# Kernel optimization log

Measured on AMD Instinct MI355X. Metric: run time of the kernel, lower is better.

Reference implementation:

```python
import jax, jax.numpy as jnp
import numpy as np

N = 200000   # 10000 graphs x 20 nodes, stacked
E = 3200000  # avg degree 16
F_IN = 4
H = 32
BN_EPS = 1e-5


def setup_inputs() -> dict:
    key = jax.random.key(0)
    ks = jax.random.split(key, 16)
    s = 0.1
    return {
        "x": jax.random.normal(ks[0], (N, F_IN), jnp.float32),
        "edge_index": jax.random.randint(ks[1], (2, E), 0, N, jnp.int64),
        "edge_weight": jax.random.uniform(ks[2], (E,), jnp.float32),
        "gcn1_w": jax.random.normal(ks[3], (F_IN, H), jnp.float32) * s,
        "gcn1_b": jnp.zeros((H,), jnp.float32),
        "gcn2_w": jax.random.normal(ks[4], (H, H), jnp.float32) * s,
        "gcn2_b": jnp.zeros((H,), jnp.float32),
        "bn1_gamma": jnp.ones((H,), jnp.float32),
        "bn1_beta": jnp.zeros((H,), jnp.float32),
        "bn1_mean": jnp.zeros((H,), jnp.float32),
        "bn1_var": jnp.ones((H,), jnp.float32),
        "bn2_gamma": jnp.ones((H,), jnp.float32),
        "bn2_beta": jnp.zeros((H,), jnp.float32),
        "bn2_mean": jnp.zeros((H,), jnp.float32),
        "bn2_var": jnp.ones((H,), jnp.float32),
        "lstm1_wih": jax.random.normal(ks[5], (4 * H, 2 * H), jnp.float32) * s,
        "lstm1_whh": jax.random.normal(ks[6], (4 * H, H), jnp.float32) * s,
        "lstm1_bih": jax.random.normal(ks[7], (4 * H,), jnp.float32) * s,
        "lstm1_bhh": jax.random.normal(ks[8], (4 * H,), jnp.float32) * s,
        "lstm2_wih": jax.random.normal(ks[9], (4 * H, H), jnp.float32) * s,
        "lstm2_whh": jax.random.normal(ks[10], (4 * H, H), jnp.float32) * s,
        "lstm2_bih": jax.random.normal(ks[11], (4 * H,), jnp.float32) * s,
        "lstm2_bhh": jax.random.normal(ks[12], (4 * H,), jnp.float32) * s,
        "lin_w": jax.random.normal(ks[13], (1, 2 * H + F_IN), jnp.float32) * s,
        "lin_b": jnp.zeros((1,), jnp.float32),
    }


def _gcn_conv(x, src, dst, ew, W, b, n):
    # GCNConv: x @ W, add self-loops (weight 1), symmetric normalization, scatter-add at dst.
    xw = x @ W
    loop = jnp.arange(n)
    s = jnp.concatenate([src, loop])
    d = jnp.concatenate([dst, loop])
    w = jnp.concatenate([ew, jnp.ones((n,), ew.dtype)])
    deg = jax.ops.segment_sum(w, d, num_segments=n)
    dinv = jnp.where(deg > 0, jax.lax.rsqrt(deg), 0.0)
    norm = dinv[s] * w * dinv[d]  # [E+N]
    out = jax.ops.segment_sum(norm[:, None] * xw[s], d, num_segments=n)
    return out + b


def _bn_eval(x, gamma, beta, mean, var):
    return (x - mean) * jax.lax.rsqrt(var + BN_EPS) * gamma + beta


def _lstm_step(x, wih, bih, bhh):
    # single timestep, zero initial (h, c): recurrent W_hh term vanishes.
    gates = x @ wih.T + bih + bhh
    i, f, g, o = jnp.split(gates, 4, axis=1)  # torch gate order i,f,g,o
    c = jax.nn.sigmoid(i) * jnp.tanh(g)
    return jax.nn.sigmoid(o) * jnp.tanh(c)


def reference(x, edge_index, edge_weight, gcn1_w, gcn1_b, gcn2_w, gcn2_b,
              bn1_gamma, bn1_beta, bn1_mean, bn1_var,
              bn2_gamma, bn2_beta, bn2_mean, bn2_var,
              lstm1_wih, lstm1_whh, lstm1_bih, lstm1_bhh,
              lstm2_wih, lstm2_whh, lstm2_bih, lstm2_bhh,
              lin_w, lin_b):
    n = x.shape[0]
    src, dst = edge_index[0], edge_index[1]
    # MPNNLSTM (window=1, eval mode: dropout=identity, BN uses running stats)
    h1 = _bn_eval(jax.nn.relu(_gcn_conv(x, src, dst, edge_weight, gcn1_w, gcn1_b, n)),
                  bn1_gamma, bn1_beta, bn1_mean, bn1_var)
    h2 = _bn_eval(jax.nn.relu(_gcn_conv(h1, src, dst, edge_weight, gcn2_w, gcn2_b, n)),
                  bn2_gamma, bn2_beta, bn2_mean, bn2_var)
    skip = jnp.concatenate([h1, h2], axis=1)  # [N, 2H]
    H1 = _lstm_step(skip, lstm1_wih, lstm1_bih, lstm1_bhh)  # [N, H]
    H2 = _lstm_step(H1, lstm2_wih, lstm2_bih, lstm2_bhh)    # [N, H]
    h = jnp.concatenate([H1, H2, x], axis=1)  # [N, 2H + F_IN]
    # RecurrentGCN head: relu + linear -> [N, 1]
    return jax.nn.relu(h) @ lin_w.T + lin_b
```

## Files before the change

kernel.cpp:

```cpp
#include <hip/hip_runtime.h>
#include <hip/hip_fp16.h>
#include <math.h>

#define BN_EPS 1e-5f
#define HF 32
#define BS 256
#define KEDGE 4096
#define MAXNB 800
#define SCAP 5504
#define WQ14 16383.0f
#define WQ22 4194303.0f

typedef _Float16 half8 __attribute__((ext_vector_type(8)));
typedef float f32x4 __attribute__((ext_vector_type(4)));
typedef float f32x2 __attribute__((ext_vector_type(2)));

__device__ __forceinline__ float fsig(float x) {
    return __builtin_amdgcn_rcpf(1.0f + __expf(-x));
}
__device__ __forceinline__ float ftanh(float x) {
    return 1.0f - 2.0f * __builtin_amdgcn_rcpf(1.0f + __expf(2.0f * x));
}


__device__ __forceinline__ float e4m3_to_f32_sw(unsigned v) {
    unsigned s = v & 0x80u, E = (v >> 3) & 0xFu, m = v & 7u;
    float r = E ? ldexpf((float)(8 + m), (int)E - 10) : ldexpf((float)m, -9);
    return s ? -r : r;
}

__device__ __forceinline__ unsigned f32_to_e4m3_sw(float x) {
    float ax = fabsf(x);
    unsigned s = x < 0.0f ? 0x80u : 0u;
    if (!(ax > 0.0f)) return s;
    if (ax >= 448.0f) return s | 0x7Eu;
    int e;
    float m = frexpf(ax, &e);
    int E = e - 1 + 7;
    if (E >= 1) {
        int q = (int)(m * 16.0f + 0.5f);
        if (q == 16) { q = 8; E += 1; if (E > 15) return s | 0x7Eu; }
        return s | (unsigned)(E << 3) | (unsigned)(q - 8);
    }
    int q = (int)(ax * 512.0f + 0.5f);
    if (q > 7) return s | 0x08u;
    return s | (unsigned)q;
}

__device__ __forceinline__ void dec8(uint2 r, float* f) {
#if __has_builtin(__builtin_amdgcn_cvt_pk_f32_fp8)
    f32x2 p0 = __builtin_amdgcn_cvt_pk_f32_fp8((int)r.x, false);
    f32x2 p1 = __builtin_amdgcn_cvt_pk_f32_fp8((int)r.x, true);
    f32x2 p2 = __builtin_amdgcn_cvt_pk_f32_fp8((int)r.y, false);
    f32x2 p3 = __builtin_amdgcn_cvt_pk_f32_fp8((int)r.y, true);
    f[0] = p0[0]; f[1] = p0[1]; f[2] = p1[0]; f[3] = p1[1];
    f[4] = p2[0]; f[5] = p2[1]; f[6] = p3[0]; f[7] = p3[1];
#else
#pragma unroll
    for (int k = 0; k < 4; ++k) f[k] = e4m3_to_f32_sw((r.x >> (8 * k)) & 0xFFu);
#pragma unroll
    for (int k = 0; k < 4; ++k) f[4 + k] = e4m3_to_f32_sw((r.y >> (8 * k)) & 0xFFu);
#endif
}

__device__ __forceinline__ uint2 enc8(const float* o) {
#if __has_builtin(__builtin_amdgcn_cvt_pk_fp8_f32)
    int w0 = 0, w1 = 0;
    w0 = __builtin_amdgcn_cvt_pk_fp8_f32(o[0], o[1], w0, false);
    w0 = __builtin_amdgcn_cvt_pk_fp8_f32(o[2], o[3], w0, true);
    w1 = __builtin_amdgcn_cvt_pk_fp8_f32(o[4], o[5], w1, false);
    w1 = __builtin_amdgcn_cvt_pk_fp8_f32(o[6], o[7], w1, true);
    return make_uint2((unsigned)w0, (unsigned)w1);
#else
    unsigned a = 0, b = 0;
#pragma unroll
    for (int k = 0; k < 4; ++k) a |= f32_to_e4m3_sw(o[k]) << (8 * k);
#pragma unroll
    for (int k = 0; k < 4; ++k) b |= f32_to_e4m3_sw(o[4 + k]) << (8 * k);
    return make_uint2(a, b);
#endif
}


__global__ __launch_bounds__(512) void k_binsort(
        const int* __restrict__ src, const int* __restrict__ dst,
        const float* __restrict__ ew, int E, int NB, int bcap,
        int* __restrict__ gcur, uint2* __restrict__ recs) {
    __shared__ int hist[MAXNB], curs[MAXNB];

    int tid = threadIdx.x;
    int base = blockIdx.x * KEDGE;
    int cnt = min(KEDGE, E - base);

    for (int i = tid; i < NB; i += 512) hist[i] = 0;
    __syncthreads();

    uint2 rec[8];
    int eb = base + tid * 8;
    int rem = cnt - tid * 8;
    if (rem >= 8) {
        int4 s0 = *(const int4*)(src + eb);
        int4 s1 = *(const int4*)(src + eb + 4);
        int4 d0 = *(const int4*)(dst + eb);
        int4 d1 = *(const int4*)(dst + eb + 4);
        float4 w0 = *(const float4*)(ew + eb);
        float4 w1 = *(const float4*)(ew + eb + 4);
        int ss[8] = {s0.x, s0.y, s0.z, s0.w, s1.x, s1.y, s1.z, s1.w};
        int dd[8] = {d0.x, d0.y, d0.z, d0.w, d1.x, d1.y, d1.z, d1.w};
        float ww[8] = {w0.x, w0.y, w0.z, w0.w, w1.x, w1.y, w1.z, w1.w};
#pragma unroll
        for (int k = 0; k < 8; ++k) {
            unsigned q = (unsigned)(ww[k] * WQ22 + 0.5f);
            if (q > 4194303u) q = 4194303u;
            int b = dd[k] >> 8;
            rec[k] = make_uint2(((unsigned)ss[k] << 8) | (unsigned)(dd[k] & 255),
                                ((unsigned)b << 22) | q);
        }
    } else {
#pragma unroll
        for (int k = 0; k < 8; ++k) {
            if (k < rem) {
                int s = src[eb + k];
                int d = dst[eb + k];
                float w = ew[eb + k];
                unsigned q = (unsigned)(w * WQ22 + 0.5f);
                if (q > 4194303u) q = 4194303u;
                int b = d >> 8;
                rec[k] = make_uint2(((unsigned)s << 8) | (unsigned)(d & 255),
                                    ((unsigned)b << 22) | q);
            }
        }
    }
#pragma unroll
    for (int k = 0; k < 8; ++k)
        if (k < rem) atomicAdd(&hist[rec[k].y >> 22], 1);
    __syncthreads();

    for (int b = tid; b < NB; b += 512) {
        int len = hist[b];
        curs[b] = len ? atomicAdd(&gcur[b], len) : 0;
    }
    __syncthreads();

#pragma unroll
    for (int k = 0; k < 8; ++k) {
        if (k < rem) {
            uint2 u = rec[k];
            int b = u.y >> 22;
            int off = atomicAdd(&curs[b], 1);
            if (off < bcap) recs[(size_t)b * bcap + off] = u;
        }
    }
}


__global__ __launch_bounds__(1024) void k_sortb(
        const uint2* __restrict__ recs, const int* __restrict__ gcur,
        int bcap, int bcap4,
        const float* __restrict__ x, const float* __restrict__ W1,
        unsigned* __restrict__ recs4, int* __restrict__ pstart,
        int* __restrict__ pcnt, float* __restrict__ dinv,
        unsigned char* __restrict__ y18,
        const float* __restrict__ wih1, const float* __restrict__ bih1,
        const float* __restrict__ bhh1, const float* __restrict__ wih2,
        const float* __restrict__ bih2, const float* __restrict__ bhh2,
        __half* __restrict__ wp1, __half* __restrict__ wp2,
        float* __restrict__ bsum1, float* __restrict__ bsum2, int n) {
    __shared__ uint2 srec[SCAP];
    __shared__ int hist[BS], excl4[BS], curs[BS], wsm[BS];
    __shared__ float sdv[BS];
    __shared__ float sW1[128];

    int b = blockIdx.x, tid = threadIdx.x;
    int cnt = min(gcur[b], bcap);
    const uint2* r = recs + (size_t)b * bcap;
    const float dq = 1.0f / WQ22;

    if (b == 0) {
        const int tg[6] = {0, 16, 64, 80, 96, 112};
        for (int idx = tid; idx < 9472; idx += 1024) {
            if (idx < 6144) {
                int t = idx >> 10, rm = idx & 1023;
                int kc = rm >> 9, rm2 = rm & 511;
                int lane = rm2 >> 3, j = rm2 & 7;
                int g = tg[t] + (lane & 15);
                int k = kc * 32 + (lane >> 4) * 8 + j;
                wp1[idx] = __float2half(wih1[g * 64 + k]);
            } else if (idx < 9216) {
                int i2 = idx - 6144;
                int t = i2 >> 9, rm2 = i2 & 511;
                int lane = rm2 >> 3, j = rm2 & 7;
                int g = tg[t] + (lane & 15);
                int k = (lane >> 4) * 8 + j;
                wp2[i2] = __float2half(wih2[g * 32 + k]);
            } else if (idx < 9344) {
                int i = idx - 9216;
                bsum1[i] = bih1[i] + bhh1[i];
            } else {
                int i = idx - 9344;
                bsum2[i] = bih2[i] + bhh2[i];
            }
        }
    }

    if (tid < BS) { hist[tid] = 0; wsm[tid] = 0; }
    if (tid >= 256 && tid < 384) sW1[tid - 256] = W1[tid - 256];
    __syncthreads();

    for (int i = tid; i < cnt; i += 1024) {
        uint2 u = r[i];
        if (i < SCAP) srec[i] = u;
        int dl = u.x & 255;
        atomicAdd(&hist[dl], 1);
        atomicAdd(&wsm[dl], (int)(u.y & 4194303u));
    }
    __syncthreads();

    if (tid < BS) {
        int g = b * BS + tid;
        sdv[tid] = (g < n) ? rsqrtf(1.0f + (float)wsm[tid] * dq) : 0.0f;
    }
    if (tid < 64) {
        int run = 0;
        for (int c = 0; c < BS; c += 64) {
            int idx = c + tid;
            int v = (hist[idx] + 3) & ~3;
            int incl = v;
#pragma unroll
            for (int o = 1; o < 64; o <<= 1) {
                int up = __shfl_up(incl, o, 64);
                if (tid >= o) incl += up;
            }
            int e = run + incl - v;
            excl4[idx] = e; curs[idx] = e;
            run += __shfl(incl, 63, 64);
        }
    }
    __syncthreads();

    unsigned* out4 = recs4 + (size_t)b * bcap4;
    for (int i = tid; i < cnt; i += 1024) {
        uint2 u = (i < SCAP) ? srec[i] : r[i];
        int dl = u.x & 255;
        int pos = atomicAdd(&curs[dl], 1);
        float qn = (float)(u.y & 4194303u) * dq * sdv[dl];
        unsigned q = (unsigned)(qn * WQ14 + 0.5f);
        if (q > 16383u) q = 16383u;
        out4[pos] = ((u.x >> 8) << 14) | q;
    }

    {
        int node = tid >> 2, q = tid & 3;
        int g = b * BS + node;
        if (g < n) {
            float4 xv = *(const float4*)(x + (size_t)g * 4);
            float sc = sdv[node];
            int f0 = q * 8;
            float o[8];
#pragma unroll
            for (int k = 0; k < 8; ++k)
                o[k] = sc * (xv.x * sW1[f0 + k] + xv.y * sW1[32 + f0 + k] +
                             xv.z * sW1[64 + f0 + k] + xv.w * sW1[96 + f0 + k]);
            ((uint2*)(y18 + ((size_t)g << 5)))[q] = enc8(o);
        }
    }

    if (tid < BS) {
        int g = b * BS + tid;
        if (g < n) {
            pstart[g] = b * bcap4 + excl4[tid];
            pcnt[g] = hist[tid];
            dinv[g] = sdv[tid];
        }
    }
}


__global__ __launch_bounds__(256) void k_g1w2(
        const unsigned* __restrict__ recs4, const int* __restrict__ pstart,
        const int* __restrict__ pcnt, const float* __restrict__ dinv,
        const unsigned char* __restrict__ y18, const float* __restrict__ W2,
        const float* __restrict__ bias, const float* __restrict__ gamma,
        const float* __restrict__ beta, const float* __restrict__ mean,
        const float* __restrict__ var,
        __half* __restrict__ skiph, unsigned char* __restrict__ A8, int n) {
    __shared__ float sW2[1024];
    __shared__ float sh1[64][33];
    int tid = threadIdx.x;
    for (int i = tid; i < 1024; i += 256) sW2[i] = W2[i];
    __syncthreads();

    int nl = tid >> 2;
    int g = blockIdx.x * 64 + nl;
    int lane = tid & 3;
    int fq = lane * 8;
    bool act = g < n;

    float acc[8];
#pragma unroll
    for (int k = 0; k < 8; ++k) acc[k] = 0.0f;

    float dig = 0.0f;
    if (act) {
        dig = dinv[g];
        {
            uint2 sr = ((const uint2*)(y18 + ((size_t)g << 5)))[lane];
            float f[8];
            dec8(sr, f);
#pragma unroll
            for (int k = 0; k < 8; ++k) acc[k] = dig * f[k];
        }

        const float qs = 1.0f / WQ14;
        int cn = pcnt[g];
        const unsigned* r = recs4 + pstart[g];
        uint4 na, nb;
        if (8 <= cn) { na = *(const uint4*)(r); nb = *(const uint4*)(r + 4); }
        int e = 0;
        for (; e + 8 <= cn; e += 8) {
            uint4 ua = na, ub = nb;
            if (e + 16 <= cn) { na = *(const uint4*)(r + e + 8); nb = *(const uint4*)(r + e + 12); }
            unsigned u[8] = {ua.x, ua.y, ua.z, ua.w, ub.x, ub.y, ub.z, ub.w};
            uint2 rw[8];
#pragma unroll
            for (int q = 0; q < 8; ++q)
                rw[q] = ((const uint2*)(y18 + ((size_t)(u[q] >> 14) << 5)))[lane];
            float nm[8];
#pragma unroll
            for (int q = 0; q < 8; ++q)
                nm[q] = (float)(u[q] & 16383u) * qs;
#pragma unroll
            for (int q = 0; q < 8; ++q) {
                float f[8];
                dec8(rw[q], f);
#pragma unroll
                for (int k = 0; k < 8; ++k) acc[k] += nm[q] * f[k];
            }
        }
        for (; e < cn; ++e) {
            unsigned u0 = r[e];
            uint2 r0 = ((const uint2*)(y18 + ((size_t)(u0 >> 14) << 5)))[lane];
            float n0 = (float)(u0 & 16383u) * qs;
            float f[8];
            dec8(r0, f);
#pragma unroll
            for (int k = 0; k < 8; ++k) acc[k] += n0 * f[k];
        }
    }

    float o[8];
#pragma unroll
    for (int k = 0; k < 8; ++k) {
        float v = fmaxf(acc[k] + bias[fq + k], 0.0f);
        o[k] = (v - mean[fq + k]) * gamma[fq + k] * rsqrtf(var[fq + k] + BN_EPS) + beta[fq + k];
        sh1[nl][fq + k] = o[k];
    }
    if (act) {
        union { __half h[8]; uint4 q; } hv;
#pragma unroll
        for (int k = 0; k < 8; ++k) hv.h[k] = __float2half(o[k]);
        *(uint4*)(skiph + (size_t)g * 32 + fq) = hv.q;
    }
    __syncthreads();

    if (act) {
        float a2[8];
#pragma unroll
        for (int j = 0; j < 8; ++j) a2[j] = 0.0f;
#pragma unroll 4
        for (int k = 0; k < 32; ++k) {
            float h = sh1[nl][k];
            const float* wr = sW2 + k * 32 + fq;
#pragma unroll
            for (int j = 0; j < 8; ++j) a2[j] += h * wr[j];
        }
#pragma unroll
        for (int j = 0; j < 8; ++j) a2[j] *= dig;
        ((uint2*)(A8 + ((size_t)g << 5)))[lane] = enc8(a2);
    }
}


__global__ __launch_bounds__(256) void k_g2head(
        const unsigned* __restrict__ recs4, const int* __restrict__ pstart,
        const int* __restrict__ pcnt, const float* __restrict__ dinv,
        const unsigned char* __restrict__ A8,
        const float* __restrict__ bias, const float* __restrict__ gamma,
        const float* __restrict__ beta, const float* __restrict__ mean,
        const float* __restrict__ var,
        const __half* __restrict__ skiph, const float* __restrict__ x,
        const __half* __restrict__ wp1, const __half* __restrict__ wp2,
        const float* __restrict__ bsum1, const float* __restrict__ bsum2,
        const float* __restrict__ lw, const float* __restrict__ lb,
        float* __restrict__ out, int n) {
    __shared__ __align__(16) __half h2s[64][40];
    __shared__ __align__(16) __half H1lds[4 * 16 * 40];
    int tid = threadIdx.x;
    int nl = tid >> 2;
    int g = blockIdx.x * 64 + nl;
    int lane = tid & 3;
    int fq = lane * 8;
    bool act = g < n;

    float acc[8];
#pragma unroll
    for (int k = 0; k < 8; ++k) acc[k] = 0.0f;

    if (act) {
        float dig = dinv[g];
        {
            uint2 sr = ((const uint2*)(A8 + ((size_t)g << 5)))[lane];
            float f[8];
            dec8(sr, f);
#pragma unroll
            for (int k = 0; k < 8; ++k) acc[k] = dig * f[k];
        }

        const float qs = 1.0f / WQ14;
        int cn = pcnt[g];
        const unsigned* r = recs4 + pstart[g];
        uint4 na, nb;
        if (8 <= cn) { na = *(const uint4*)(r); nb = *(const uint4*)(r + 4); }
        int e = 0;
        for (; e + 8 <= cn; e += 8) {
            uint4 ua = na, ub = nb;
            if (e + 16 <= cn) { na = *(const uint4*)(r + e + 8); nb = *(const uint4*)(r + e + 12); }
            unsigned u[8] = {ua.x, ua.y, ua.z, ua.w, ub.x, ub.y, ub.z, ub.w};
            uint2 rw[8];
#pragma unroll
            for (int q = 0; q < 8; ++q)
                rw[q] = ((const uint2*)(A8 + ((size_t)(u[q] >> 14) << 5)))[lane];
            float nm[8];
#pragma unroll
            for (int q = 0; q < 8; ++q)
                nm[q] = (float)(u[q] & 16383u) * qs;
#pragma unroll
            for (int q = 0; q < 8; ++q) {
                float f[8];
                dec8(rw[q], f);
#pragma unroll
                for (int k = 0; k < 8; ++k) acc[k] += nm[q] * f[k];
            }
        }
        for (; e < cn; ++e) {
            unsigned u0 = r[e];
            uint2 r0 = ((const uint2*)(A8 + ((size_t)(u0 >> 14) << 5)))[lane];
            float n0 = (float)(u0 & 16383u) * qs;
            float f0[8];
            dec8(r0, f0);
#pragma unroll
            for (int k = 0; k < 8; ++k) acc[k] += n0 * f0[k];
        }

        union { __half h[8]; uint4 q; } hv;
#pragma unroll
        for (int k = 0; k < 8; ++k) {
            float v = fmaxf(acc[k] + bias[fq + k], 0.0f);
            hv.h[k] = __float2half((v - mean[fq + k]) * gamma[fq + k] *
                                   rsqrtf(var[fq + k] + BN_EPS) + beta[fq + k]);
        }
        *(uint4*)(&h2s[nl][fq]) = hv.q;
    }
    __syncthreads();

    int w = tid >> 6, l = tid & 63;
    int quad = l >> 4, c = l & 15;
    int node_base = blockIdx.x * 64 + w * 16;

    int arow = node_base + c; if (arow > n - 1) arow = n - 1;
    int lr = arow - blockIdx.x * 64;
    half8 a0 = *(const half8*)(skiph + (size_t)arow * 32 + quad * 8);
    half8 a1 = *(const half8*)(&h2s[lr][quad * 8]);

    const half8* b1 = (const half8*)wp1;
    f32x4 d[6];
#pragma unroll
    for (int t = 0; t < 6; ++t) {
        f32x4 ac = {0.0f, 0.0f, 0.0f, 0.0f};
        ac = __builtin_amdgcn_mfma_f32_16x16x32_f16(a0, b1[(t * 2 + 0) * 64 + l], ac, 0, 0, 0);
        ac = __builtin_amdgcn_mfma_f32_16x16x32_f16(a1, b1[(t * 2 + 1) * 64 + l], ac, 0, 0, 0);
        d[t] = ac;
    }

    float bi0 = bsum1[c],      bi1 = bsum1[16 + c];
    float bg0 = bsum1[64 + c], bg1 = bsum1[80 + c];
    float bo0 = bsum1[96 + c], bo1 = bsum1[112 + c];
    float lwc0 = lw[c], lwc1 = lw[c + 16];

    float pa[4];
#pragma unroll
    for (int r = 0; r < 4; ++r) {
        float cc0 = fsig(d[0][r] + bi0) * ftanh(d[2][r] + bg0);
        float h0 = fsig(d[4][r] + bo0) * ftanh(cc0);
        float cc1 = fsig(d[1][r] + bi1) * ftanh(d[3][r] + bg1);
        float h1 = fsig(d[5][r] + bo1) * ftanh(cc1);
        pa[r] = fmaxf(h0, 0.0f) * lwc0 + fmaxf(h1, 0.0f) * lwc1;
        __half* hp = H1lds + (w * 16 + quad * 4 + r) * 40;
        hp[c] = __float2half(h0);
        hp[c + 16] = __float2half(h1);
    }
    __syncthreads();

    half8 a2 = *(const half8*)(H1lds + (w * 16 + c) * 40 + quad * 8);

    const half8* b2 = (const half8*)wp2;
    f32x4 e2[6];
#pragma unroll
    for (int t = 0; t < 6; ++t) {
        f32x4 ac = {0.0f, 0.0f, 0.0f, 0.0f};
        e2[t] = __builtin_amdgcn_mfma_f32_16x16x32_f16(a2, b2[t * 64 + l], ac, 0, 0, 0);
    }

    float ci0 = bsum2[c],      ci1 = bsum2[16 + c];
    float cg0 = bsum2[64 + c], cg1 = bsum2[80 + c];
    float co0 = bsum2[96 + c], co1 = bsum2[112 + c];
    float lw2c0 = lw[32 + c], lw2c1 = lw[48 + c];
#pragma unroll
    for (int r = 0; r < 4; ++r) {
        float cc0 = fsig(e2[0][r] + ci0) * ftanh(e2[2][r] + cg0);
        float h0 = fsig(e2[4][r] + co0) * ftanh(cc0);
        float cc1 = fsig(e2[1][r] + ci1) * ftanh(e2[3][r] + cg1);
        float h1 = fsig(e2[5][r] + co1) * ftanh(cc1);
        pa[r] += fmaxf(h0, 0.0f) * lw2c0 + fmaxf(h1, 0.0f) * lw2c1;
    }

#pragma unroll
    for (int m = 1; m < 16; m <<= 1) {
#pragma unroll
        for (int r = 0; r < 4; ++r) pa[r] += __shfl_xor(pa[r], m, 64);
    }

    if (c < 4) {
        int node = node_base + quad * 4 + c;
        if (node < n) {
            const float4 xv = *(const float4*)(x + (size_t)node * 4);
            out[node] = pa[c] + lb[0]
                + fmaxf(xv.x, 0.0f) * lw[64] + fmaxf(xv.y, 0.0f) * lw[65]
                + fmaxf(xv.z, 0.0f) * lw[66] + fmaxf(xv.w, 0.0f) * lw[67];
        }
    }
}


__global__ void k_initdeg(float* __restrict__ deg, int n) {
    int i = blockIdx.x * blockDim.x + threadIdx.x;
    if (i < n) deg[i] = 1.0f;
}

__global__ void k_deg_only(const int* __restrict__ dst, const float* __restrict__ ew,
                           float* __restrict__ deg, int E) {
    int e = blockIdx.x * blockDim.x + threadIdx.x;
    if (e < E) atomicAdd(&deg[dst[e]], ew[e]);
}

__global__ void k_dinv_f(float* __restrict__ deg, int n) {
    int i = blockIdx.x * blockDim.x + threadIdx.x;
    if (i < n) {
        float d = deg[i];
        deg[i] = d > 0.0f ? rsqrtf(d) : 0.0f;
    }
}

__global__ void k_xw1_f(const float* __restrict__ x, const float* __restrict__ W,
                        float* __restrict__ out, int n) {
    int idx = blockIdx.x * blockDim.x + threadIdx.x;
    if (idx >= n * HF) return;
    int nn = idx >> 5, f = idx & 31;
    const float4 xr = *(const float4*)(x + (size_t)nn * 4);
    out[idx] = xr.x * W[f] + xr.y * W[32 + f] + xr.z * W[64 + f] + xr.w * W[96 + f];
}

__global__ void k_xw2_f(const float* __restrict__ Hin, const float* __restrict__ W,
                        float* __restrict__ out, int n) {
    __shared__ float sW[32 * 32];
    __shared__ float sH[8][32];
    int tid = threadIdx.x;
    for (int i = tid; i < 1024; i += 256) sW[i] = W[i];
    int r = tid >> 5, f = tid & 31;
    int nn = blockIdx.x * 8 + r;
    if (nn < n) sH[r][f] = Hin[(size_t)nn * HF + f];
    __syncthreads();
    if (nn >= n) return;
    float acc = 0.0f;
#pragma unroll
    for (int k = 0; k < 32; ++k) acc += sH[r][k] * sW[k * 32 + f];
    out[(size_t)nn * HF + f] = acc;
}

__global__ void k_selfloop(const float* __restrict__ A, const float* __restrict__ dinv,
                           float* __restrict__ B, int n) {
    int idx = blockIdx.x * blockDim.x + threadIdx.x;
    if (idx >= n * HF) return;
    int nn = idx >> 5;
    float di = dinv[nn];
    B[idx] = di * di * A[idx];
}

__global__ void k_scatter(const int* __restrict__ src, const int* __restrict__ dst,
                          const float* __restrict__ ew, const float* __restrict__ dinv,
                          const float* __restrict__ A, float* __restrict__ B, int total) {
    int idx = blockIdx.x * blockDim.x + threadIdx.x;
    if (idx >= total) return;
    int e = idx >> 5, f = idx & 31;
    int s = src[e], d = dst[e];
    float norm = dinv[s] * ew[e] * dinv[d];
    atomicAdd(&B[d * HF + f], norm * A[s * HF + f]);
}

__global__ void k_post(const float* __restrict__ B, const float* __restrict__ bias,
                       const float* __restrict__ gamma, const float* __restrict__ beta,
                       const float* __restrict__ mean, const float* __restrict__ var,
                       float* __restrict__ Hout, int n) {
    int idx = blockIdx.x * blockDim.x + threadIdx.x;
    if (idx >= n * HF) return;
    int f = idx & 31;
    float v = fmaxf(B[idx] + bias[f], 0.0f);
    float sc = gamma[f] * rsqrtf(var[f] + BN_EPS);
    Hout[idx] = (v - mean[f]) * sc + beta[f];
}

__global__ __launch_bounds__(256) void k_head(
        const float* __restrict__ h1, const float* __restrict__ h2,
        const float* __restrict__ x,
        const float* __restrict__ wih1, const float* __restrict__ bih1, const float* __restrict__ bhh1,
        const float* __restrict__ wih2, const float* __restrict__ bih2, const float* __restrict__ bhh2,
        const float* __restrict__ lw, const float* __restrict__ lb,
        float* __restrict__ out, int n) {
    __shared__ float sH1[32 * 256];
    int tid = threadIdx.x;
    int nn = blockIdx.x * 256 + tid;
    if (nn >= n) return;

    const float4* a = (const float4*)(h1 + (size_t)nn * HF);
    const float4* b = (const float4*)(h2 + (size_t)nn * HF);
    float skip[64];
#pragma unroll
    for (int q = 0; q < 8; ++q) {
        float4 v = a[q];
        skip[4 * q] = v.x; skip[4 * q + 1] = v.y; skip[4 * q + 2] = v.z; skip[4 * q + 3] = v.w;
        float4 u = b[q];
        skip[32 + 4 * q] = u.x; skip[33 + 4 * q] = u.y; skip[34 + 4 * q] = u.z; skip[35 + 4 * q] = u.w;
    }

    float oa = lb[0];
#pragma unroll 1
    for (int j = 0; j < 32; ++j) {
        const float4* wi = (const float4*)(wih1 + (size_t)j * 64);
        const float4* wg = (const float4*)(wih1 + (size_t)(64 + j) * 64);
        const float4* wo = (const float4*)(wih1 + (size_t)(96 + j) * 64);
        float gi = bih1[j] + bhh1[j];
        float gg = bih1[64 + j] + bhh1[64 + j];
        float go = bih1[96 + j] + bhh1[96 + j];
#pragma unroll
        for (int q = 0; q < 16; ++q) {
            float4 aa = wi[q], bb = wg[q], cc4 = wo[q];
            float s0 = skip[4 * q], s1 = skip[4 * q + 1], s2 = skip[4 * q + 2], s3 = skip[4 * q + 3];
            gi += aa.x * s0 + aa.y * s1 + aa.z * s2 + aa.w * s3;
            gg += bb.x * s0 + bb.y * s1 + bb.z * s2 + bb.w * s3;
            go += cc4.x * s0 + cc4.y * s1 + cc4.z * s2 + cc4.w * s3;
        }
        float cc = fsig(gi) * ftanh(gg);
        float hh = fsig(go) * ftanh(cc);
        sH1[j * 256 + tid] = hh;
        oa += fmaxf(hh, 0.0f) * lw[j];
    }

#pragma unroll 1
    for (int j = 0; j < 32; ++j) {
        const float4* wi = (const float4*)(wih2 + (size_t)j * 32);
        const float4* wg = (const float4*)(wih2 + (size_t)(64 + j) * 32);
        const float4* wo = (const float4*)(wih2 + (size_t)(96 + j) * 32);
        float gi = bih2[j] + bhh2[j];
        float gg = bih2[64 + j] + bhh2[64 + j];
        float go = bih2[96 + j] + bhh2[96 + j];
#pragma unroll
        for (int q = 0; q < 8; ++q) {
            float4 aa = wi[q], bb = wg[q], cc4 = wo[q];
            float s0 = sH1[(4 * q) * 256 + tid], s1 = sH1[(4 * q + 1) * 256 + tid];
            float s2 = sH1[(4 * q + 2) * 256 + tid], s3 = sH1[(4 * q + 3) * 256 + tid];
            gi += aa.x * s0 + aa.y * s1 + aa.z * s2 + aa.w * s3;
            gg += bb.x * s0 + bb.y * s1 + bb.z * s2 + bb.w * s3;
            go += cc4.x * s0 + cc4.y * s1 + cc4.z * s2 + cc4.w * s3;
        }
        float cc = fsig(gi) * ftanh(gg);
        float hh = fsig(go) * ftanh(cc);
        oa += fmaxf(hh, 0.0f) * lw[32 + j];
    }

    const float4 xv = *(const float4*)(x + (size_t)nn * 4);
    oa += fmaxf(xv.x, 0.0f) * lw[64] + fmaxf(xv.y, 0.0f) * lw[65] +
          fmaxf(xv.z, 0.0f) * lw[66] + fmaxf(xv.w, 0.0f) * lw[67];
    out[nn] = oa;
}


extern "C" void kernel_launch(void* const* d_in, const int* in_sizes, int n_in,
                              void* d_out, int out_size, void* d_ws, size_t ws_size,
                              hipStream_t stream) {
    const float* x   = (const float*)d_in[0];
    const int*   ei  = (const int*)d_in[1];
    const float* ew  = (const float*)d_in[2];
    const float* g1w = (const float*)d_in[3];
    const float* g1b = (const float*)d_in[4];
    const float* g2w = (const float*)d_in[5];
    const float* g2b = (const float*)d_in[6];
    const float* bn1g = (const float*)d_in[7];
    const float* bn1b = (const float*)d_in[8];
    const float* bn1m = (const float*)d_in[9];
    const float* bn1v = (const float*)d_in[10];
    const float* bn2g = (const float*)d_in[11];
    const float* bn2b = (const float*)d_in[12];
    const float* bn2m = (const float*)d_in[13];
    const float* bn2v = (const float*)d_in[14];
    const float* w1ih = (const float*)d_in[15];
    const float* b1ih = (const float*)d_in[17];
    const float* b1hh = (const float*)d_in[18];
    const float* w2ih = (const float*)d_in[19];
    const float* b2ih = (const float*)d_in[21];
    const float* b2hh = (const float*)d_in[22];
    const float* lw   = (const float*)d_in[23];
    const float* lb   = (const float*)d_in[24];
    float* out = (float*)d_out;

    const int N = in_sizes[0] / 4;
    const int E = in_sizes[2];
    const int* src = ei;
    const int* dst = ei + E;

    const int T = 256;
    const int NB = (N + BS - 1) / BS;
    long long meanb = ((long long)BS * E) / (N > 0 ? N : 1);
    int bcap = (int)(meanb + meanb / 4 + 128);
    bcap = (bcap + 3) & ~3;
    int bcap4 = bcap + 3 * BS;

    char* p = (char*)d_ws;
    auto alloc = [&](size_t bytes) { char* q = p; p += (bytes + 255) & ~(size_t)255; return q; };
    int*      gcur   = (int*)alloc(sizeof(int) * NB);
    uint2*    recs   = (uint2*)alloc(sizeof(uint2) * (size_t)NB * bcap);
    unsigned* recs4  = (unsigned*)alloc(sizeof(unsigned) * (size_t)NB * bcap4);
    float*    dinv   = (float*)alloc(sizeof(float) * N);
    int*      pstart = (int*)alloc(sizeof(int) * N);
    int*      pcnt   = (int*)alloc(sizeof(int) * N);
    unsigned char* y18 = (unsigned char*)alloc((size_t)N * HF);
    unsigned char* A8  = (unsigned char*)alloc((size_t)N * HF);
    __half*   skiph  = (__half*)alloc(sizeof(__half) * (size_t)N * 32);
    __half*   wp1    = (__half*)alloc(sizeof(__half) * 6144);
    __half*   wp2    = (__half*)alloc(sizeof(__half) * 3072);
    float*    bsum1  = (float*)alloc(sizeof(float) * 128);
    float*    bsum2  = (float*)alloc(sizeof(float) * 128);
    size_t need = (size_t)(p - (char*)d_ws);

    int bN  = (N + T - 1) / T;
    int bE  = (E + T - 1) / T;
    int bNF = (N * HF + T - 1) / T;
    int bN8 = (N + 7) / 8;
    int bG  = (N + 63) / 64;
    int bBin = (E + KEDGE - 1) / KEDGE;

    if (ws_size >= need && NB <= MAXNB && N <= (1 << 18) && bcap <= SCAP) {
        hipMemsetAsync(gcur, 0, sizeof(int) * NB, stream);
        k_binsort<<<bBin, 512, 0, stream>>>(src, dst, ew, E, NB, bcap, gcur, recs);
        k_sortb<<<NB, 1024, 0, stream>>>(recs, gcur, bcap, bcap4, x, g1w,
                                         recs4, pstart, pcnt, dinv, y18,
                                         w1ih, b1ih, b1hh, w2ih, b2ih, b2hh,
                                         wp1, wp2, bsum1, bsum2, N);

        k_g1w2<<<bG, T, 0, stream>>>(recs4, pstart, pcnt, dinv, y18, g2w,
                                     g1b, bn1g, bn1b, bn1m, bn1v, skiph, A8, N);
        k_g2head<<<bG, T, 0, stream>>>(recs4, pstart, pcnt, dinv, A8,
                                       g2b, bn2g, bn2b, bn2m, bn2v,
                                       skiph, x, wp1, wp2, bsum1, bsum2,
                                       lw, lb, out, N);
    } else {
        size_t Npad = ((size_t)N + 255) & ~(size_t)255;
        float* fdinv = (float*)d_ws;
        float* fA = fdinv + Npad;
        float* fB = fA + (size_t)N * HF;
        float* fC = fB + (size_t)N * HF;
        int bEF = (int)(((long long)E * HF + T - 1) / T);
        int bH = (N + 255) / 256;

        k_initdeg<<<bN, T, 0, stream>>>(fdinv, N);
        k_deg_only<<<bE, T, 0, stream>>>(dst, ew, fdinv, E);
        k_dinv_f<<<bN, T, 0, stream>>>(fdinv, N);

        k_xw1_f<<<bNF, T, 0, stream>>>(x, g1w, fA, N);
        k_selfloop<<<bNF, T, 0, stream>>>(fA, fdinv, fB, N);
        k_scatter<<<bEF, T, 0, stream>>>(src, dst, ew, fdinv, fA, fB, E * HF);
        k_post<<<bNF, T, 0, stream>>>(fB, g1b, bn1g, bn1b, bn1m, bn1v, fC, N);

        k_xw2_f<<<bN8, T, 0, stream>>>(fC, g2w, fA, N);
        k_selfloop<<<bNF, T, 0, stream>>>(fA, fdinv, fB, N);
        k_scatter<<<bEF, T, 0, stream>>>(src, dst, ew, fdinv, fA, fB, E * HF);
        k_post<<<bNF, T, 0, stream>>>(fB, g2b, bn2g, bn2b, bn2m, bn2v, fB, N);

        k_head<<<bH, T, 0, stream>>>(fC, fB, x, w1ih, b1ih, b1hh, w2ih, b2ih, b2hh,
                                     lw, lb, out, N);
    }
}
```

Before: 294.7 us.

## Split each node's edge gather across two 4-lane groups with shuffle reduction

Both GCN aggregation kernels now assign 8 threads per node instead of 4, splitting the neighbor list into two halves (aligned to 8) processed by separate lane groups, then combining partial sums with a cross-lane shuffle. Blocks cover 32 nodes instead of 64, doubling the grid, and the gather loop is factored into a shared helper. This is meant to raise memory-level parallelism and shorten the per-thread serial gather chain. In exchange, the dense LSTM/head stage in the second kernel leaves half the block idle, and some threads get uneven work when degrees are small.

```diff
diff --git a/kernel.cpp b/kernel.cpp
--- a/kernel.cpp
+++ b/kernel.cpp
@@ -79,6 +79,44 @@
     for (int k = 0; k < 4; ++k) b |= f32_to_e4m3_sw(o[4 + k]) << (8 * k);
     return make_uint2(a, b);
 #endif
+}
+
+__device__ __forceinline__ void gather_seg(
+        const unsigned* __restrict__ r, int e0, int e1,
+        const unsigned char* __restrict__ rows, int lane, float* acc) {
+    const float qs = 1.0f / WQ14;
+    int e = e0;
+    uint4 na, nb;
+    if (e + 8 <= e1) { na = *(const uint4*)(r + e); nb = *(const uint4*)(r + e + 4); }
+    for (; e + 8 <= e1; e += 8) {
+        uint4 ua = na, ub = nb;
+        if (e + 16 <= e1) { na = *(const uint4*)(r + e + 8); nb = *(const uint4*)(r + e + 12); }
+        unsigned u[8] = {ua.x, ua.y, ua.z, ua.w, ub.x, ub.y, ub.z, ub.w};
+        uint2 rw[8];
+#pragma unroll
+        for (int q = 0; q < 8; ++q)
+            rw[q] = ((const uint2*)(rows + ((size_t)(u[q] >> 14) << 5)))[lane];
+        float nm[8];
+#pragma unroll
+        for (int q = 0; q < 8; ++q)
+            nm[q] = (float)(u[q] & 16383u) * qs;
+#pragma unroll
+        for (int q = 0; q < 8; ++q) {
+            float f[8];
+            dec8(rw[q], f);
+#pragma unroll
+            for (int k = 0; k < 8; ++k) acc[k] += nm[q] * f[k];
+        }
+    }
+    for (; e < e1; ++e) {
+        unsigned u0 = r[e];
+        uint2 r0 = ((const uint2*)(rows + ((size_t)(u0 >> 14) << 5)))[lane];
+        float n0 = (float)(u0 & 16383u) * qs;
+        float f[8];
+        dec8(r0, f);
+#pragma unroll
+        for (int k = 0; k < 8; ++k) acc[k] += n0 * f[k];
+    }
 }
 
 
@@ -285,14 +323,15 @@
         const float* __restrict__ var,
         __half* __restrict__ skiph, unsigned char* __restrict__ A8, int n) {
     __shared__ float sW2[1024];
-    __shared__ float sh1[64][33];
+    __shared__ float sh1[32][33];
     int tid = threadIdx.x;
     for (int i = tid; i < 1024; i += 256) sW2[i] = W2[i];
     __syncthreads();
 
-    int nl = tid >> 2;
-    int g = blockIdx.x * 64 + nl;
+    int nl = tid >> 3;
+    int grp = (tid >> 2) & 1;
     int lane = tid & 3;
+    int g = blockIdx.x * 32 + nl;
     int fq = lane * 8;
     bool act = g < n;
 
@@ -303,67 +342,42 @@
     float dig = 0.0f;
     if (act) {
         dig = dinv[g];
-        {
+        if (grp == 0) {
             uint2 sr = ((const uint2*)(y18 + ((size_t)g << 5)))[lane];
             float f[8];
             dec8(sr, f);
 #pragma unroll
             for (int k = 0; k < 8; ++k) acc[k] = dig * f[k];
         }
-
-        const float qs = 1.0f / WQ14;
         int cn = pcnt[g];
         const unsigned* r = recs4 + pstart[g];
-        uint4 na, nb;
-        if (8 <= cn) { na = *(const uint4*)(r); nb = *(const uint4*)(r + 4); }
-        int e = 0;
-        for (; e + 8 <= cn; e += 8) {
-            uint4 ua = na, ub = nb;
-            if (e + 16 <= cn) { na = *(const uint4*)(r + e + 8); nb = *(const uint4*)(r + e + 12); }
-            unsigned u[8] = {ua.x, ua.y, ua.z, ua.w, ub.x, ub.y, ub.z, ub.w};
-            uint2 rw[8];
-#pragma unroll
-            for (int q = 0; q < 8; ++q)
-                rw[q] = ((const uint2*)(y18 + ((size_t)(u[q] >> 14) << 5)))[lane];
-            float nm[8];
-#pragma unroll
-            for (int q = 0; q < 8; ++q)
-                nm[q] = (float)(u[q] & 16383u) * qs;
-#pragma unroll
-            for (int q = 0; q < 8; ++q) {
-                float f[8];
-                dec8(rw[q], f);
-#pragma unroll
-                for (int k = 0; k < 8; ++k) acc[k] += nm[q] * f[k];
-            }
-        }
-        for (; e < cn; ++e) {
-            unsigned u0 = r[e];
-            uint2 r0 = ((const uint2*)(y18 + ((size_t)(u0 >> 14) << 5)))[lane];
-            float n0 = (float)(u0 & 16383u) * qs;
-            float f[8];
-            dec8(r0, f);
-#pragma unroll
-            for (int k = 0; k < 8; ++k) acc[k] += n0 * f[k];
-        }
-    }
-
-    float o[8];
-#pragma unroll
-    for (int k = 0; k < 8; ++k) {
-        float v = fmaxf(acc[k] + bias[fq + k], 0.0f);
-        o[k] = (v - mean[fq + k]) * gamma[fq + k] * rsqrtf(var[fq + k] + BN_EPS) + beta[fq + k];
-        sh1[nl][fq + k] = o[k];
-    }
-    if (act) {
-        union { __half h[8]; uint4 q; } hv;
-#pragma unroll
-        for (int k = 0; k < 8; ++k) hv.h[k] = __float2half(o[k]);
-        *(uint4*)(skiph + (size_t)g * 32 + fq) = hv.q;
-    }
-    __syncthreads();
-
-    if (act) {
+        int half8 = (((cn >> 1) + 7) >> 3) << 3;
+        int e0 = grp ? min(half8, cn) : 0;
+        int e1 = grp ? cn : min(half8, cn);
+        gather_seg(r, e0, e1, y18, lane, acc);
+    }
+
+#pragma unroll
+    for (int k = 0; k < 8; ++k) acc[k] += __shfl_xor(acc[k], 4, 64);
+
+    if (grp == 0) {
+        float o[8];
+#pragma unroll
+        for (int k = 0; k < 8; ++k) {
+            float v = fmaxf(acc[k] + bias[fq + k], 0.0f);
+            o[k] = (v - mean[fq + k]) * gamma[fq + k] * rsqrtf(var[fq + k] + BN_EPS) + beta[fq + k];
+            sh1[nl][fq + k] = o[k];
+        }
+        if (act) {
+            union { __half h[8]; uint4 q; } hv;
+#pragma unroll
+            for (int k = 0; k < 8; ++k) hv.h[k] = __float2half(o[k]);
+            *(uint4*)(skiph + (size_t)g * 32 + fq) = hv.q;
+        }
+    }
+    __syncthreads();
+
+    if (grp == 0 && act) {
         float a2[8];
 #pragma unroll
         for (int j = 0; j < 8; ++j) a2[j] = 0.0f;
@@ -393,12 +407,13 @@
         const float* __restrict__ bsum1, const float* __restrict__ bsum2,
         const float* __restrict__ lw, const float* __restrict__ lb,
         float* __restrict__ out, int n) {
-    __shared__ __align__(16) __half h2s[64][40];
-    __shared__ __align__(16) __half H1lds[4 * 16 * 40];
+    __shared__ __align__(16) __half h2s[32][40];
+    __shared__ __align__(16) __half H1lds[2 * 16 * 40];
     int tid = threadIdx.x;
-    int nl = tid >> 2;
-    int g = blockIdx.x * 64 + nl;
+    int nl = tid >> 3;
+    int grp = (tid >> 2) & 1;
     int lane = tid & 3;
+    int g = blockIdx.x * 32 + nl;
     int fq = lane * 8;
     bool act = g < n;
 
@@ -408,50 +423,25 @@
 
     if (act) {
         float dig = dinv[g];
-        {
+        if (grp == 0) {
             uint2 sr = ((const uint2*)(A8 + ((size_t)g << 5)))[lane];
             float f[8];
             dec8(sr, f);
 #pragma unroll
             for (int k = 0; k < 8; ++k) acc[k] = dig * f[k];
         }
-
-        const float qs = 1.0f / WQ14;
         int cn = pcnt[g];
         const unsigned* r = recs4 + pstart[g];
-        uint4 na, nb;
-        if (8 <= cn) { na = *(const uint4*)(r); nb = *(const uint4*)(r + 4); }
-        int e = 0;
-        for (; e + 8 <= cn; e += 8) {
-            uint4 ua = na, ub = nb;
-            if (e + 16 <= cn) { na = *(const uint4*)(r + e + 8); nb = *(const uint4*)(r + e + 12); }
-            unsigned u[8] = {ua.x, ua.y, ua.z, ua.w, ub.x, ub.y, ub.z, ub.w};
-            uint2 rw[8];
-#pragma unroll
-            for (int q = 0; q < 8; ++q)
-                rw[q] = ((const uint2*)(A8 + ((size_t)(u[q] >> 14) << 5)))[lane];
-            float nm[8];
-#pragma unroll
-            for (int q = 0; q < 8; ++q)
-                nm[q] = (float)(u[q] & 16383u) * qs;
-#pragma unroll
-            for (int q = 0; q < 8; ++q) {
-                float f[8];
-                dec8(rw[q], f);
-#pragma unroll
-                for (int k = 0; k < 8; ++k) acc[k] += nm[q] * f[k];
-            }
-        }
-        for (; e < cn; ++e) {
-            unsigned u0 = r[e];
-            uint2 r0 = ((const uint2*)(A8 + ((size_t)(u0 >> 14) << 5)))[lane];
-            float n0 = (float)(u0 & 16383u) * qs;
-            float f0[8];
-            dec8(r0, f0);
-#pragma unroll
-            for (int k = 0; k < 8; ++k) acc[k] += n0 * f0[k];
-        }
-
+        int half8 = (((cn >> 1) + 7) >> 3) << 3;
+        int e0 = grp ? min(half8, cn) : 0;
+        int e1 = grp ? cn : min(half8, cn);
+        gather_seg(r, e0, e1, A8, lane, acc);
+    }
+
+#pragma unroll
+    for (int k = 0; k < 8; ++k) acc[k] += __shfl_xor(acc[k], 4, 64);
+
+    if (grp == 0 && act) {
         union { __half h[8]; uint4 q; } hv;
 #pragma unroll
         for (int k = 0; k < 8; ++k) {
@@ -465,78 +455,83 @@
 
     int w = tid >> 6, l = tid & 63;
     int quad = l >> 4, c = l & 15;
-    int node_base = blockIdx.x * 64 + w * 16;
-
-    int arow = node_base + c; if (arow > n - 1) arow = n - 1;
-    int lr = arow - blockIdx.x * 64;
-    half8 a0 = *(const half8*)(skiph + (size_t)arow * 32 + quad * 8);
-    half8 a1 = *(const half8*)(&h2s[lr][quad * 8]);
-
-    const half8* b1 = (const half8*)wp1;
-    f32x4 d[6];
-#pragma unroll
-    for (int t = 0; t < 6; ++t) {
-        f32x4 ac = {0.0f, 0.0f, 0.0f, 0.0f};
-        ac = __builtin_amdgcn_mfma_f32_16x16x32_f16(a0, b1[(t * 2 + 0) * 64 + l], ac, 0, 0, 0);
-        ac = __builtin_amdgcn_mfma_f32_16x16x32_f16(a1, b1[(t * 2 + 1) * 64 + l], ac, 0, 0, 0);
-        d[t] = ac;
-    }
-
-    float bi0 = bsum1[c],      bi1 = bsum1[16 + c];
-    float bg0 = bsum1[64 + c], bg1 = bsum1[80 + c];
-    float bo0 = bsum1[96 + c], bo1 = bsum1[112 + c];
-    float lwc0 = lw[c], lwc1 = lw[c + 16];
-
-    float pa[4];
-#pragma unroll
-    for (int r = 0; r < 4; ++r) {
-        float cc0 = fsig(d[0][r] + bi0) * ftanh(d[2][r] + bg0);
-        float h0 = fsig(d[4][r] + bo0) * ftanh(cc0);
-        float cc1 = fsig(d[1][r] + bi1) * ftanh(d[3][r] + bg1);
-        float h1 = fsig(d[5][r] + bo1) * ftanh(cc1);
-        pa[r] = fmaxf(h0, 0.0f) * lwc0 + fmaxf(h1, 0.0f) * lwc1;
-        __half* hp = H1lds + (w * 16 + quad * 4 + r) * 40;
-        hp[c] = __float2half(h0);
-        hp[c + 16] = __float2half(h1);
-    }
-    __syncthreads();
-
-    half8 a2 = *(const half8*)(H1lds + (w * 16 + c) * 40 + quad * 8);
-
-    const half8* b2 = (const half8*)wp2;
-    f32x4 e2[6];
-#pragma unroll
-    for (int t = 0; t < 6; ++t) {
-        f32x4 ac = {0.0f, 0.0f, 0.0f, 0.0f};
-        e2[t] = __builtin_amdgcn_mfma_f32_16x16x32_f16(a2, b2[t * 64 + l], ac, 0, 0, 0);
-    }
-
-    float ci0 = bsum2[c],      ci1 = bsum2[16 + c];
-    float cg0 = bsum2[64 + c], cg1 = bsum2[80 + c];
-    float co0 = bsum2[96 + c], co1 = bsum2[112 + c];
-    float lw2c0 = lw[32 + c], lw2c1 = lw[48 + c];
-#pragma unroll
-    for (int r = 0; r < 4; ++r) {
-        float cc0 = fsig(e2[0][r] + ci0) * ftanh(e2[2][r] + cg0);
-        float h0 = fsig(e2[4][r] + co0) * ftanh(cc0);
-        float cc1 = fsig(e2[1][r] + ci1) * ftanh(e2[3][r] + cg1);
-        float h1 = fsig(e2[5][r] + co1) * ftanh(cc1);
-        pa[r] += fmaxf(h0, 0.0f) * lw2c0 + fmaxf(h1, 0.0f) * lw2c1;
-    }
-
-#pragma unroll
-    for (int m = 1; m < 16; m <<= 1) {
-#pragma unroll
-        for (int r = 0; r < 4; ++r) pa[r] += __shfl_xor(pa[r], m, 64);
-    }
-
-    if (c < 4) {
-        int node = node_base + quad * 4 + c;
-        if (node < n) {
-            const float4 xv = *(const float4*)(x + (size_t)node * 4);
-            out[node] = pa[c] + lb[0]
-                + fmaxf(xv.x, 0.0f) * lw[64] + fmaxf(xv.y, 0.0f) * lw[65]
-                + fmaxf(xv.z, 0.0f) * lw[66] + fmaxf(xv.w, 0.0f) * lw[67];
+    int node_base = blockIdx.x * 32 + w * 16;
+    bool hact = tid < 128;
+
+    float pa[4] = {0.0f, 0.0f, 0.0f, 0.0f};
+    if (hact) {
+        int arow = node_base + c; if (arow > n - 1) arow = n - 1;
+        int lr = arow - blockIdx.x * 32;
+        half8 a0 = *(const half8*)(skiph + (size_t)arow * 32 + quad * 8);
+        half8 a1 = *(const half8*)(&h2s[lr][quad * 8]);
+
+        const half8* b1 = (const half8*)wp1;
+        f32x4 d[6];
+#pragma unroll
+        for (int t = 0; t < 6; ++t) {
+            f32x4 ac = {0.0f, 0.0f, 0.0f, 0.0f};
+            ac = __builtin_amdgcn_mfma_f32_16x16x32_f16(a0, b1[(t * 2 + 0) * 64 + l], ac, 0, 0, 0);
+            ac = __builtin_amdgcn_mfma_f32_16x16x32_f16(a1, b1[(t * 2 + 1) * 64 + l], ac, 0, 0, 0);
+            d[t] = ac;
+        }
+
+        float bi0 = bsum1[c],      bi1 = bsum1[16 + c];
+        float bg0 = bsum1[64 + c], bg1 = bsum1[80 + c];
+        float bo0 = bsum1[96 + c], bo1 = bsum1[112 + c];
+        float lwc0 = lw[c], lwc1 = lw[c + 16];
+
+#pragma unroll
+        for (int r = 0; r < 4; ++r) {
+            float cc0 = fsig(d[0][r] + bi0) * ftanh(d[2][r] + bg0);
+            float h0 = fsig(d[4][r] + bo0) * ftanh(cc0);
+            float cc1 = fsig(d[1][r] + bi1) * ftanh(d[3][r] + bg1);
+            float h1 = fsig(d[5][r] + bo1) * ftanh(cc1);
+            pa[r] = fmaxf(h0, 0.0f) * lwc0 + fmaxf(h1, 0.0f) * lwc1;
+            __half* hp = H1lds + (w * 16 + quad * 4 + r) * 40;
+            hp[c] = __float2half(h0);
+            hp[c + 16] = __float2half(h1);
+        }
+    }
+    __syncthreads();
+
+    if (hact) {
+        half8 a2 = *(const half8*)(H1lds + (w * 16 + c) * 40 + quad * 8);
+
+        const half8* b2 = (const half8*)wp2;
+        f32x4 e2[6];
+#pragma unroll
+        for (int t = 0; t < 6; ++t) {
+            f32x4 ac = {0.0f, 0.0f, 0.0f, 0.0f};
+            e2[t] = __builtin_amdgcn_mfma_f32_16x16x32_f16(a2, b2[t * 64 + l], ac, 0, 0, 0);
+        }
+
+        float ci0 = bsum2[c],      ci1 = bsum2[16 + c];
+        float cg0 = bsum2[64 + c], cg1 = bsum2[80 + c];
+        float co0 = bsum2[96 + c], co1 = bsum2[112 + c];
+        float lw2c0 = lw[32 + c], lw2c1 = lw[48 + c];
+#pragma unroll
+        for (int r = 0; r < 4; ++r) {
+            float cc0 = fsig(e2[0][r] + ci0) * ftanh(e2[2][r] + cg0);
+            float h0 = fsig(e2[4][r] + co0) * ftanh(cc0);
+            float cc1 = fsig(e2[1][r] + ci1) * ftanh(e2[3][r] + cg1);
+            float h1 = fsig(e2[5][r] + co1) * ftanh(cc1);
+            pa[r] += fmaxf(h0, 0.0f) * lw2c0 + fmaxf(h1, 0.0f) * lw2c1;
+        }
+
+#pragma unroll
+        for (int m = 1; m < 16; m <<= 1) {
+#pragma unroll
+            for (int r = 0; r < 4; ++r) pa[r] += __shfl_xor(pa[r], m, 64);
+        }
+
+        if (c < 4) {
+            int node = node_base + quad * 4 + c;
+            if (node < n) {
+                const float4 xv = *(const float4*)(x + (size_t)node * 4);
+                out[node] = pa[c] + lb[0]
+                    + fmaxf(xv.x, 0.0f) * lw[64] + fmaxf(xv.y, 0.0f) * lw[65]
+                    + fmaxf(xv.z, 0.0f) * lw[66] + fmaxf(xv.w, 0.0f) * lw[67];
+            }
         }
     }
 }
@@ -755,7 +750,7 @@
     int bE  = (E + T - 1) / T;
     int bNF = (N * HF + T - 1) / T;
     int bN8 = (N + 7) / 8;
-    int bG  = (N + 63) / 64;
+    int bG32 = (N + 31) / 32;
     int bBin = (E + KEDGE - 1) / KEDGE;
 
     if (ws_size >= need && NB <= MAXNB && N <= (1 << 18) && bcap <= SCAP) {
@@ -766,12 +761,12 @@
                                          w1ih, b1ih, b1hh, w2ih, b2ih, b2hh,
                                          wp1, wp2, bsum1, bsum2, N);
 
-        k_g1w2<<<bG, T, 0, stream>>>(recs4, pstart, pcnt, dinv, y18, g2w,
-                                     g1b, bn1g, bn1b, bn1m, bn1v, skiph, A8, N);
-        k_g2head<<<bG, T, 0, stream>>>(recs4, pstart, pcnt, dinv, A8,
-                                       g2b, bn2g, bn2b, bn2m, bn2v,
-                                       skiph, x, wp1, wp2, bsum1, bsum2,
-                                       lw, lb, out, N);
+        k_g1w2<<<bG32, T, 0, stream>>>(recs4, pstart, pcnt, dinv, y18, g2w,
+                                       g1b, bn1g, bn1b, bn1m, bn1v, skiph, A8, N);
+        k_g2head<<<bG32, T, 0, stream>>>(recs4, pstart, pcnt, dinv, A8,
+                                         g2b, bn2g, bn2b, bn2m, bn2v,
+                                         skiph, x, wp1, wp2, bsum1, bsum2,
+                                         lw, lb, out, N);
     } else {
         size_t Npad = ((size_t)N + 255) & ~(size_t)255;
         float* fdinv = (float*)d_ws;
```

Result: slower. 320.9 us (+8.9%).
